# Kernel optimization log

Measured on AMD Instinct MI355X. Metric: run time of the kernel, lower is better.

Reference implementation:

```python
import jax, jax.numpy as jnp
import numpy as np

N = 4194304  # number of sampled points (flattened)
W = 32       # hidden width
IN_PTS, IN_VIEWS = 3, 3


def setup_inputs() -> dict:
    key = jax.random.key(0)
    ks = jax.random.split(key, 13)
    def lin(k, fan_in, fan_out):
        # torch nn.Linear default init: U(-1/sqrt(fan_in), 1/sqrt(fan_in))
        bound = 1.0 / np.sqrt(fan_in)
        kw, kb = jax.random.split(k)
        w = jax.random.uniform(kw, (fan_in, fan_out), jnp.float32, -bound, bound)
        b = jax.random.uniform(kb, (fan_out,), jnp.float32, -bound, bound)
        return w, b
    x = jax.random.normal(ks[0], (N, IN_PTS + IN_VIEWS), jnp.float32)
    w0, b0 = lin(ks[1], IN_PTS, W)          # pts_linears[0]
    w1, b1 = lin(ks[2], W, W)               # pts_linears[1]
    wf, bf = lin(ks[3], W, W)               # feature_linear
    ws, bs = lin(ks[4], W, 1)               # sigma_linear
    wv, bv = lin(ks[5], IN_VIEWS + W, W)    # view_linears[0]
    wr, br = lin(ks[6], W, 3)               # rgb_linear
    return {"x": x, "w0": w0, "b0": b0, "w1": w1, "b1": b1,
            "wf": wf, "bf": bf, "ws": ws, "bs": bs,
            "wv": wv, "bv": bv, "wr": wr, "br": br}


def reference(x, w0, b0, w1, b1, wf, bf, ws, bs, wv, bv, wr, br):
    pts, views = x[..., :IN_PTS], x[..., IN_PTS:]
    h = jax.nn.relu(pts @ w0 + b0)
    h = jax.nn.relu(h @ w1 + b1)
    sigma = h @ ws + bs                     # [N, 1]
    feature = h @ wf + bf                   # [N, W]
    h = jnp.concatenate([feature, views], axis=-1)  # [N, W+3]
    h = jax.nn.relu(h @ wv + bv)
    rgb = h @ wr + br                       # [N, 3]
    return jnp.concatenate([rgb, sigma], axis=-1)   # [N, 4]
```

## Files before the change

kernel.cpp:

```cpp
#include <hip/hip_runtime.h>


#define NPTS   4194304
#define NT32   (NPTS / 32)

typedef _Float16 f16;
typedef _Float16 f16x2 __attribute__((ext_vector_type(2)));
typedef _Float16 f16x8 __attribute__((ext_vector_type(8)));
typedef float    f32x16 __attribute__((ext_vector_type(16)));

union H8 { f16x8 v; unsigned u[4]; };

static __device__ __forceinline__ unsigned pkrtz(float a, float b) {
    return __builtin_bit_cast(unsigned, __builtin_amdgcn_cvt_pkrtz(a, b));
}
static __device__ __forceinline__ unsigned relu2(unsigned w) {
    f16x2 h = __builtin_bit_cast(f16x2, w);
    f16x2 z = (f16x2)(f16)0.f;
    return __builtin_bit_cast(unsigned, __builtin_elementwise_max(h, z));
}

#define MFMA32(A, B, C) __builtin_amdgcn_mfma_f32_32x32x16_f16((A), (B), (C), 0, 0, 0)

__global__ __launch_bounds__(256, 4) void kilonerf_m32(
    const float* __restrict__ x,
    const float* __restrict__ w0, const float* __restrict__ b0,
    const float* __restrict__ w1, const float* __restrict__ b1,
    const float* __restrict__ wf, const float* __restrict__ bf,
    const float* __restrict__ ws, const float* __restrict__ bs,
    const float* __restrict__ wv, const float* __restrict__ bv,
    const float* __restrict__ wr, const float* __restrict__ br,
    float* __restrict__ out)
{
    const int lane = threadIdx.x & 63;
    const int m  = lane & 31;
    const int hi = lane >> 5;

    int sj[8], row[16];
#pragma unroll
    for (int j = 0; j < 8; ++j)  sj[j]  = (j & 3) + 8 * (j >> 2) + 4 * hi;
#pragma unroll
    for (int r = 0; r < 16; ++r) row[r] = (r & 3) + 8 * (r >> 2) + 4 * hi;

    float bve = bv[m];
#pragma unroll 8
    for (int k = 0; k < 32; ++k) bve = fmaf(wv[k * 32 + m], bf[k], bve);

    f16x8 aw0x, awv2x, aw1lo, aw1hi, awflo, awfhi, awvlo, awvhi, awrlo, awrhi;
#pragma unroll
    for (int j = 0; j < 8; ++j) {
        const int k = sj[j];
        aw0x[j]  = (k < 3) ? (f16)w0[k * 32 + m]
                  : (k == 3 ? (f16)b0[m] : (f16)0.f);
        awv2x[j] = (k >= 4 && k < 7) ? (f16)wv[(32 + (k - 4)) * 32 + m]
                  : (k == 7 ? (f16)bve : (f16)0.f);
        aw1lo[j] = (f16)w1[k * 32 + m];
        aw1hi[j] = (f16)w1[(16 + k) * 32 + m];
        awflo[j] = (f16)wf[k * 32 + m];
        awfhi[j] = (f16)wf[(16 + k) * 32 + m];
        awvlo[j] = (f16)wv[k * 32 + m];
        awvhi[j] = (f16)wv[(16 + k) * 32 + m];
        awrlo[j] = (m < 3) ? (f16)wr[k * 3 + m] : (f16)0.f;
        awrhi[j] = (m < 3) ? (f16)wr[(16 + k) * 3 + m] : (f16)0.f;
    }

    float wsv[16];
    f32x16 b1c;
#pragma unroll
    for (int r = 0; r < 16; ++r) {
        wsv[r] = ws[row[r]];
        b1c[r] = b1[row[r]];
    }

    const float br0 = br[0], br1 = br[1], br2 = br[2], bs0 = bs[0];

    f32x16 zf;
#pragma unroll
    for (int r = 0; r < 16; ++r) zf[r] = 0.f;

    const int wslot  = blockIdx.x * 4 + (threadIdx.x >> 6);
    const int nslots = gridDim.x * 4;

    for (int tile = wslot; tile < NT32; tile += nslots) {
        const float2* xp2 = reinterpret_cast<const float2*>(
            x + (size_t)(tile * 32 + m) * 6);
        const float2 a0 = xp2[0], a1 = xp2[1], a2 = xp2[2];

        const float fa = hi ? a1.y : a0.x;
        const float fb = hi ? a2.x : a0.y;
        const float fc = hi ? a2.y : a1.x;
        H8 bx;
        bx.u[0] = pkrtz(fa, fb);
        bx.u[1] = pkrtz(fc, 1.0f);
        bx.u[2] = 0u;
        bx.u[3] = 0u;

        f32x16 c0 = MFMA32(aw0x, bx.v, zf);
        f32x16 cv = MFMA32(awv2x, bx.v, zf);

        H8 blo, bhi;
        blo.u[0] = relu2(pkrtz(c0[0], c0[1]));
        blo.u[1] = relu2(pkrtz(c0[2], c0[3]));
        blo.u[2] = relu2(pkrtz(c0[4], c0[5]));
        blo.u[3] = relu2(pkrtz(c0[6], c0[7]));
        bhi.u[0] = relu2(pkrtz(c0[8], c0[9]));
        bhi.u[1] = relu2(pkrtz(c0[10], c0[11]));
        bhi.u[2] = relu2(pkrtz(c0[12], c0[13]));
        bhi.u[3] = relu2(pkrtz(c0[14], c0[15]));

        f32x16 c1 = MFMA32(aw1lo, blo.v, b1c);
        c1 = MFMA32(aw1hi, bhi.v, c1);

        float s0 = 0.f, s1 = 0.f, s2 = 0.f, s3 = 0.f;
#pragma unroll
        for (int r = 0; r < 4; ++r) {
            s0 = fmaf(fmaxf(c1[r],      0.f), wsv[r],      s0);
            s1 = fmaf(fmaxf(c1[4 + r],  0.f), wsv[4 + r],  s1);
            s2 = fmaf(fmaxf(c1[8 + r],  0.f), wsv[8 + r],  s2);
            s3 = fmaf(fmaxf(c1[12 + r], 0.f), wsv[12 + r], s3);
        }
        float sg = (s0 + s1) + (s2 + s3);
        sg += __shfl_xor(sg, 32);

        blo.u[0] = relu2(pkrtz(c1[0], c1[1]));
        blo.u[1] = relu2(pkrtz(c1[2], c1[3]));
        blo.u[2] = relu2(pkrtz(c1[4], c1[5]));
        blo.u[3] = relu2(pkrtz(c1[6], c1[7]));
        bhi.u[0] = relu2(pkrtz(c1[8], c1[9]));
        bhi.u[1] = relu2(pkrtz(c1[10], c1[11]));
        bhi.u[2] = relu2(pkrtz(c1[12], c1[13]));
        bhi.u[3] = relu2(pkrtz(c1[14], c1[15]));

        f32x16 cf = MFMA32(awflo, blo.v, zf);
        cf = MFMA32(awfhi, bhi.v, cf);

        blo.u[0] = pkrtz(cf[0], cf[1]);
        blo.u[1] = pkrtz(cf[2], cf[3]);
        blo.u[2] = pkrtz(cf[4], cf[5]);
        blo.u[3] = pkrtz(cf[6], cf[7]);
        bhi.u[0] = pkrtz(cf[8], cf[9]);
        bhi.u[1] = pkrtz(cf[10], cf[11]);
        bhi.u[2] = pkrtz(cf[12], cf[13]);
        bhi.u[3] = pkrtz(cf[14], cf[15]);

        cv = MFMA32(awvlo, blo.v, cv);
        cv = MFMA32(awvhi, bhi.v, cv);

        blo.u[0] = relu2(pkrtz(cv[0], cv[1]));
        blo.u[1] = relu2(pkrtz(cv[2], cv[3]));
        blo.u[2] = relu2(pkrtz(cv[4], cv[5]));
        blo.u[3] = relu2(pkrtz(cv[6], cv[7]));
        bhi.u[0] = relu2(pkrtz(cv[8], cv[9]));
        bhi.u[1] = relu2(pkrtz(cv[10], cv[11]));
        bhi.u[2] = relu2(pkrtz(cv[12], cv[13]));
        bhi.u[3] = relu2(pkrtz(cv[14], cv[15]));

        f32x16 cr = MFMA32(awrlo, blo.v, zf);
        cr = MFMA32(awrhi, bhi.v, cr);

        if (hi == 0) {
            float4 o = make_float4(cr[0] + br0, cr[1] + br1,
                                   cr[2] + br2, sg + bs0);
            *reinterpret_cast<float4*>(out + (size_t)(tile * 32 + m) * 4) = o;
        }
    }
}

extern "C" void kernel_launch(void* const* d_in, const int* in_sizes, int n_in,
                              void* d_out, int out_size, void* d_ws, size_t ws_size,
                              hipStream_t stream) {
    const float* x  = (const float*)d_in[0];
    const float* w0 = (const float*)d_in[1];
    const float* b0 = (const float*)d_in[2];
    const float* w1 = (const float*)d_in[3];
    const float* b1 = (const float*)d_in[4];
    const float* wf = (const float*)d_in[5];
    const float* bf = (const float*)d_in[6];
    const float* ws = (const float*)d_in[7];
    const float* bs = (const float*)d_in[8];
    const float* wv = (const float*)d_in[9];
    const float* bv = (const float*)d_in[10];
    const float* wr = (const float*)d_in[11];
    const float* br = (const float*)d_in[12];
    float* out = (float*)d_out;

    dim3 block(256);
    dim3 grid(2048);
    kilonerf_m32<<<grid, block, 0, stream>>>(x, w0, b0, w1, b1, wf, bf,
                                             ws, bs, wv, bv, wr, br, out);
}
```

Before: 62.66 us.

## Fold feature and view linear weights into one product; prefetch next tile inputs

The feature layer has no activation, so Wf·Wv is precomputed per thread in the prologue and applied as one 32x32 MFMA pair, with bf folded into the view bias. This removes two MFMAs and a round of fp32→fp16 packing per tile. The inputs for the next tile are also loaded one iteration ahead in registers to hide global load latency. The prologue gains a 32-term dot product per weight element, and register pressure rises.

```diff
diff --git a/kernel.cpp b/kernel.cpp
--- a/kernel.cpp
+++ b/kernel.cpp
@@ -22,7 +22,7 @@
 
 #define MFMA32(A, B, C) __builtin_amdgcn_mfma_f32_32x32x16_f16((A), (B), (C), 0, 0, 0)
 
-__global__ __launch_bounds__(256, 4) void kilonerf_m32(
+__global__ __launch_bounds__(256, 4) void kilonerf_r12(
     const float* __restrict__ x,
     const float* __restrict__ w0, const float* __restrict__ b0,
     const float* __restrict__ w1, const float* __restrict__ b1,
@@ -46,7 +46,7 @@
 #pragma unroll 8
     for (int k = 0; k < 32; ++k) bve = fmaf(wv[k * 32 + m], bf[k], bve);
 
-    f16x8 aw0x, awv2x, aw1lo, aw1hi, awflo, awfhi, awvlo, awvhi, awrlo, awrhi;
+    f16x8 aw0x, awv2x, aw1lo, aw1hi, awclo, awchi, awrlo, awrhi;
 #pragma unroll
     for (int j = 0; j < 8; ++j) {
         const int k = sj[j];
@@ -56,10 +56,14 @@
                   : (k == 7 ? (f16)bve : (f16)0.f);
         aw1lo[j] = (f16)w1[k * 32 + m];
         aw1hi[j] = (f16)w1[(16 + k) * 32 + m];
-        awflo[j] = (f16)wf[k * 32 + m];
-        awfhi[j] = (f16)wf[(16 + k) * 32 + m];
-        awvlo[j] = (f16)wv[k * 32 + m];
-        awvhi[j] = (f16)wv[(16 + k) * 32 + m];
+        float wc0 = 0.f, wc1 = 0.f;
+#pragma unroll 8
+        for (int t = 0; t < 32; ++t) {
+            wc0 = fmaf(wf[k * 32 + t],        wv[t * 32 + m], wc0);
+            wc1 = fmaf(wf[(16 + k) * 32 + t], wv[t * 32 + m], wc1);
+        }
+        awclo[j] = (f16)wc0;
+        awchi[j] = (f16)wc1;
         awrlo[j] = (m < 3) ? (f16)wr[k * 3 + m] : (f16)0.f;
         awrhi[j] = (m < 3) ? (f16)wr[(16 + k) * 3 + m] : (f16)0.f;
     }
@@ -81,14 +85,22 @@
     const int wslot  = blockIdx.x * 4 + (threadIdx.x >> 6);
     const int nslots = gridDim.x * 4;
 
+    float2 cx0, cx1, cx2;
+    {
+        const float2* xp2 = reinterpret_cast<const float2*>(
+            x + (size_t)(wslot * 32 + m) * 6);
+        cx0 = xp2[0]; cx1 = xp2[1]; cx2 = xp2[2];
+    }
+
     for (int tile = wslot; tile < NT32; tile += nslots) {
-        const float2* xp2 = reinterpret_cast<const float2*>(
-            x + (size_t)(tile * 32 + m) * 6);
-        const float2 a0 = xp2[0], a1 = xp2[1], a2 = xp2[2];
+        int np = tile + nslots; if (np >= NT32) np = wslot;
+        const float2* xn = reinterpret_cast<const float2*>(
+            x + (size_t)(np * 32 + m) * 6);
+        float2 nx0 = xn[0], nx1 = xn[1], nx2 = xn[2];
 
-        const float fa = hi ? a1.y : a0.x;
-        const float fb = hi ? a2.x : a0.y;
-        const float fc = hi ? a2.y : a1.x;
+        const float fa = hi ? cx1.y : cx0.x;
+        const float fb = hi ? cx2.x : cx0.y;
+        const float fc = hi ? cx2.y : cx1.x;
         H8 bx;
         bx.u[0] = pkrtz(fa, fb);
         bx.u[1] = pkrtz(fc, 1.0f);
@@ -131,29 +143,17 @@
         bhi.u[2] = relu2(pkrtz(c1[12], c1[13]));
         bhi.u[3] = relu2(pkrtz(c1[14], c1[15]));
 
-        f32x16 cf = MFMA32(awflo, blo.v, zf);
-        cf = MFMA32(awfhi, bhi.v, cf);
+        f32x16 cc = MFMA32(awclo, blo.v, cv);
+        cc = MFMA32(awchi, bhi.v, cc);
 
-        blo.u[0] = pkrtz(cf[0], cf[1]);
-        blo.u[1] = pkrtz(cf[2], cf[3]);
-        blo.u[2] = pkrtz(cf[4], cf[5]);
-        blo.u[3] = pkrtz(cf[6], cf[7]);
-        bhi.u[0] = pkrtz(cf[8], cf[9]);
-        bhi.u[1] = pkrtz(cf[10], cf[11]);
-        bhi.u[2] = pkrtz(cf[12], cf[13]);
-        bhi.u[3] = pkrtz(cf[14], cf[15]);
-
-        cv = MFMA32(awvlo, blo.v, cv);
-        cv = MFMA32(awvhi, bhi.v, cv);
-
-        blo.u[0] = relu2(pkrtz(cv[0], cv[1]));
-        blo.u[1] = relu2(pkrtz(cv[2], cv[3]));
-        blo.u[2] = relu2(pkrtz(cv[4], cv[5]));
-        blo.u[3] = relu2(pkrtz(cv[6], cv[7]));
-        bhi.u[0] = relu2(pkrtz(cv[8], cv[9]));
-        bhi.u[1] = relu2(pkrtz(cv[10], cv[11]));
-        bhi.u[2] = relu2(pkrtz(cv[12], cv[13]));
-        bhi.u[3] = relu2(pkrtz(cv[14], cv[15]));
+        blo.u[0] = relu2(pkrtz(cc[0], cc[1]));
+        blo.u[1] = relu2(pkrtz(cc[2], cc[3]));
+        blo.u[2] = relu2(pkrtz(cc[4], cc[5]));
+        blo.u[3] = relu2(pkrtz(cc[6], cc[7]));
+        bhi.u[0] = relu2(pkrtz(cc[8], cc[9]));
+        bhi.u[1] = relu2(pkrtz(cc[10], cc[11]));
+        bhi.u[2] = relu2(pkrtz(cc[12], cc[13]));
+        bhi.u[3] = relu2(pkrtz(cc[14], cc[15]));
 
         f32x16 cr = MFMA32(awrlo, blo.v, zf);
         cr = MFMA32(awrhi, bhi.v, cr);
@@ -163,6 +163,8 @@
                                    cr[2] + br2, sg + bs0);
             *reinterpret_cast<float4*>(out + (size_t)(tile * 32 + m) * 4) = o;
         }
+
+        cx0 = nx0; cx1 = nx1; cx2 = nx2;
     }
 }
 
@@ -186,6 +188,6 @@
 
     dim3 block(256);
     dim3 grid(2048);
-    kilonerf_m32<<<grid, block, 0, stream>>>(x, w0, b0, w1, b1, wf, bf,
+    kilonerf_r12<<<grid, block, 0, stream>>>(x, w0, b0, w1, b1, wf, bf,
                                              ws, bs, wv, bv, wr, br, out);
 }
```

New measurement: 94.63 us. +51.0%, slower.
